# Optimization experiments

Hardware: AMD Instinct MI355X
Metric: run time of the kernel (lower is better)

Reference implementation:

```python
import jax, jax.numpy as jnp
import numpy as np

B, S, D, H = 8, 1024, 1024, 16
DK = D // H  # 64


def setup_inputs() -> dict:
    key = jax.random.key(0)
    ks = jax.random.split(key, 12)
    def w(k):
        return (jax.random.normal(k, (D, D), dtype=jnp.float32) * 0.02)
    def b(k):
        return (jax.random.normal(k, (D,), dtype=jnp.float32) * 0.02)
    return {
        "q": jax.random.normal(ks[0], (B, S, D), dtype=jnp.float32),
        "k": jax.random.normal(ks[1], (B, S, D), dtype=jnp.float32),
        "v": jax.random.normal(ks[2], (B, S, D), dtype=jnp.float32),
        "mask": jax.random.randint(ks[3], (B, 1, S, S), 0, 2, dtype=jnp.int32),
        "WQ_w": w(ks[4]), "WQ_b": b(ks[5]),
        "WK_w": w(ks[6]), "WK_b": b(ks[7]),
        "WV_w": w(ks[8]), "WV_b": b(ks[9]),
        "WO_w": w(ks[10]), "WO_b": b(ks[11]),
    }


def reference(q, k, v, mask, WQ_w, WQ_b, WK_w, WK_b, WV_w, WV_b, WO_w, WO_b):
    # nn.Linear: y = x @ W.T + b
    Q = (q @ WQ_w.T + WQ_b).reshape(B, S, H, DK)
    K = (k @ WK_w.T + WK_b).reshape(B, S, H, DK)
    V = (v @ WV_w.T + WV_b).reshape(B, S, H, DK)
    # scores: [B, H, Sq, Sk]
    scores = jnp.einsum("bqhd,bkhd->bhqk", Q, K) / jnp.sqrt(jnp.float32(DK))
    scores = jnp.where(mask == 0, jnp.float32(-1e9), scores)
    attn = jax.nn.softmax(scores, axis=-1)
    # dropout p=0.0 -> identity
    out = jnp.einsum("bhqk,bkhd->bqhd", attn, V).reshape(B, S, D)
    return out @ WO_w.T + WO_b
```

## Files before the change

### kernel.cpp

```cpp
#include <hip/hip_runtime.h>
#include <math.h>

typedef __bf16 bf16;
typedef __bf16 bf16x8 __attribute__((ext_vector_type(8)));
typedef __bf16 bf16x4 __attribute__((ext_vector_type(4)));
typedef float f32x2 __attribute__((ext_vector_type(2)));
typedef float f32x4 __attribute__((ext_vector_type(4)));
typedef float f32x16 __attribute__((ext_vector_type(16)));
typedef int i32x4 __attribute__((ext_vector_type(4)));

constexpr int B_ = 8, S_ = 1024, D_ = 1024, H_ = 16, DK_ = 64;
constexpr int M_ = B_ * S_;
constexpr size_t A8 = (size_t)1 << 23;
constexpr size_t W1 = (size_t)1 << 20;
constexpr float QSCALE = 0.18033688011112042f;

#if __has_builtin(__builtin_amdgcn_exp2f)
#define EXP2F(x) __builtin_amdgcn_exp2f(x)
#else
#define EXP2F(x) exp2f(x)
#endif
#if __has_builtin(__builtin_amdgcn_rcpf)
#define RCPF(x) __builtin_amdgcn_rcpf(x)
#else
#define RCPF(x) (1.0f / (x))
#endif

#define GAS(p) ((const __attribute__((address_space(1))) void*)(p))
#define LAS(p) ((__attribute__((address_space(3))) void*)(p))

__device__ __forceinline__ float xor32f(float v, int bpidx) {
    return __builtin_bit_cast(float,
        __builtin_amdgcn_ds_bpermute(bpidx, __builtin_bit_cast(int, v)));
}
__device__ __forceinline__ int xor32i(int v, int bpidx) {
    return __builtin_amdgcn_ds_bpermute(bpidx, v);
}
__device__ __forceinline__ int pack_bf16(bf16 lo, bf16 hi) {
    return (int)(unsigned)__builtin_bit_cast(unsigned short, lo)
         | ((int)(unsigned)__builtin_bit_cast(unsigned short, hi) << 16);
}

struct F4Q { f32x4 a, b, c, d; };


__global__ __launch_bounds__(256) void cvt_all(
    const float* __restrict__ q, const float* __restrict__ k,
    const float* __restrict__ v, const float* __restrict__ w0,
    const float* __restrict__ w1, const float* __restrict__ w2,
    const float* __restrict__ w3, bf16* __restrict__ dst)
{
    size_t e = ((size_t)blockIdx.x * 256 + threadIdx.x) * 8;
    const float* src;
    size_t off;
    if (e < 3 * A8) {
        int t = (int)(e >> 23);
        src = (t == 0) ? q : (t == 1) ? k : v;
        off = e & (A8 - 1);
    } else {
        size_t ew = e - 3 * A8;
        int t = (int)(ew >> 20);
        src = (t == 0) ? w0 : (t == 1) ? w1 : (t == 2) ? w2 : w3;
        off = ew & (W1 - 1);
    }
    float4 a = *(const float4*)(src + off);
    float4 b = *(const float4*)(src + off + 4);
    bf16x8 o = { (bf16)a.x, (bf16)a.y, (bf16)a.z, (bf16)a.w,
                 (bf16)b.x, (bf16)b.y, (bf16)b.z, (bf16)b.w };
    *(bf16x8*)(dst + e) = o;
}

__global__ __launch_bounds__(256) void mask_cvt(
    const int* __restrict__ mask, float* __restrict__ mf)
{
    const int bx = blockIdx.x;
    const int kt = bx & 15, qt = (bx >> 4) & 7, b = bx >> 7;
    const int tid = threadIdx.x;
    const int w = tid >> 6, lane = tid & 63;
    const int hi = lane >> 5, l31 = lane & 31;
    const int q = qt * 128 + w * 32 + l31;

    const int* src = mask + ((size_t)b << 20) + (size_t)q * 1024 + kt * 64 + hi * 4;
    float* dst = mf + (size_t)bx * 8192 + w * 2048 + lane * 4;
#pragma unroll
    for (int blk = 0; blk < 2; ++blk)
#pragma unroll
        for (int rr = 0; rr < 4; ++rr) {
            int4 m = *(const int4*)(src + blk * 32 + rr * 8);
            f32x4 o = { m.x ? 0.f : -1e9f, m.y ? 0.f : -1e9f,
                        m.z ? 0.f : -1e9f, m.w ? 0.f : -1e9f };
            *(f32x4*)(dst + (blk * 4 + rr) * 256) = o;
        }
}

__global__ __launch_bounds__(256) void qkv_gemm(
    const bf16* __restrict__ qb, const bf16* __restrict__ kb,
    const bf16* __restrict__ vb, const bf16* __restrict__ wq,
    const bf16* __restrict__ wk, const bf16* __restrict__ wv,
    const float* __restrict__ bq, const float* __restrict__ bk,
    const float* __restrict__ bv, bf16* __restrict__ Qp,
    bf16* __restrict__ Kp, bf16* __restrict__ Vp, float qscale)
{
    constexpr int K = 1024;
    __shared__ bf16 As[128 * 32];
    __shared__ bf16 Bs[128 * 32];

    const int bid = blockIdx.x;
    const int which = bid >> 9;
    const int gb = bid & 511;
    const bf16* X = which == 0 ? qb : which == 1 ? kb : vb;
    const bf16* W = which == 0 ? wq : which == 1 ? wk : wv;
    const float* bias = which == 0 ? bq : which == 1 ? bk : bv;
    bf16* outp = which == 0 ? Qp : which == 1 ? Kp : Vp;
    const float oscale = which == 0 ? qscale : 1.0f;

    const int tid  = threadIdx.x;
    const int lane = tid & 63;
    const int w    = tid >> 6;
    const int wm   = w & 1, wn = w >> 1;
    const int quad = lane >> 4, l15 = lane & 15;
    const int bm = (gb & 63) * 128, bn = (gb >> 6) * 128;

    f32x4 acc[4][4];
#pragma unroll
    for (int i = 0; i < 4; ++i)
#pragma unroll
        for (int j = 0; j < 4; ++j)
#pragma unroll
            for (int r = 0; r < 4; ++r) acc[i][j][r] = 0.f;

    const int lrow = lane >> 2;
    const int lcol = (lane & 3) * 8;

    for (int k0 = 0; k0 < K; k0 += 32) {
        __syncthreads();
#pragma unroll
        for (int i = 0; i < 2; ++i) {
            const int rbase = w * 16 + i * 64;
            __builtin_amdgcn_global_load_lds(
                GAS(X + (size_t)(bm + rbase + lrow) * K + k0 + lcol),
                LAS(As + rbase * 32), 16, 0, 0);
            __builtin_amdgcn_global_load_lds(
                GAS(W + (size_t)(bn + rbase + lrow) * K + k0 + lcol),
                LAS(Bs + rbase * 32), 16, 0, 0);
        }
        __syncthreads();

        bf16x8 a[4], b[4];
#pragma unroll
        for (int i = 0; i < 4; ++i)
            a[i] = *(const bf16x8*)(As + (wm * 64 + i * 16 + l15) * 32 + quad * 8);
#pragma unroll
        for (int j = 0; j < 4; ++j)
            b[j] = *(const bf16x8*)(Bs + (wn * 64 + j * 16 + l15) * 32 + quad * 8);
#pragma unroll
        for (int i = 0; i < 4; ++i)
#pragma unroll
            for (int j = 0; j < 4; ++j)
                acc[i][j] = __builtin_amdgcn_mfma_f32_16x16x32_bf16(
                    a[i], b[j], acc[i][j], 0, 0, 0);
    }

#pragma unroll
    for (int i = 0; i < 4; ++i) {
#pragma unroll
        for (int j = 0; j < 4; ++j) {
            const int n = bn + wn * 64 + j * 16 + l15;
            const float bs = bias[n];
            if (which == 2) {
                const int m0 = bm + wm * 64 + i * 16 + quad * 4;
                const int bb = m0 >> 10, s0 = m0 & 1023;
                const int h = n >> 6, dk = n & 63;
                bf16x4 o;
#pragma unroll
                for (int r = 0; r < 4; ++r) o[r] = (bf16)(acc[i][j][r] + bs);
                *(bf16x4*)(outp + (((size_t)(bb * 16 + h) * 64 + dk) << 10) + s0) = o;
            } else {
#pragma unroll
                for (int r = 0; r < 4; ++r) {
                    const int m = bm + wm * 64 + i * 16 + quad * 4 + r;
                    const int bb = m >> 10, s = m & 1023;
                    const int h = n >> 6, dk = n & 63;
                    outp[(((size_t)(bb * 16 + h)) * 1024 + s) * 64 + dk] =
                        (bf16)((acc[i][j][r] + bs) * oscale);
                }
            }
        }
    }
}

__global__ __launch_bounds__(256) void gemm_out(
    const bf16* __restrict__ X, const bf16* __restrict__ W,
    const float* __restrict__ bias, float* __restrict__ outv)
{
    constexpr int K = 1024;
    __shared__ bf16 As[128 * 32];
    __shared__ bf16 Bs[128 * 32];

    const int tid  = threadIdx.x;
    const int lane = tid & 63;
    const int w    = tid >> 6;
    const int wm   = w & 1, wn = w >> 1;
    const int quad = lane >> 4, l15 = lane & 15;
    const int bm = blockIdx.x * 128, bn = blockIdx.y * 128;

    f32x4 acc[4][4];
#pragma unroll
    for (int i = 0; i < 4; ++i)
#pragma unroll
        for (int j = 0; j < 4; ++j)
#pragma unroll
            for (int r = 0; r < 4; ++r) acc[i][j][r] = 0.f;

    const int lrow = lane >> 2;
    const int lcol = (lane & 3) * 8;

    for (int k0 = 0; k0 < K; k0 += 32) {
        __syncthreads();
#pragma unroll
        for (int i = 0; i < 2; ++i) {
            const int rbase = w * 16 + i * 64;
            __builtin_amdgcn_global_load_lds(
                GAS(X + (size_t)(bm + rbase + lrow) * K + k0 + lcol),
                LAS(As + rbase * 32), 16, 0, 0);
            __builtin_amdgcn_global_load_lds(
                GAS(W + (size_t)(bn + rbase + lrow) * K + k0 + lcol),
                LAS(Bs + rbase * 32), 16, 0, 0);
        }
        __syncthreads();

        bf16x8 a[4], b[4];
#pragma unroll
        for (int i = 0; i < 4; ++i)
            a[i] = *(const bf16x8*)(As + (wm * 64 + i * 16 + l15) * 32 + quad * 8);
#pragma unroll
        for (int j = 0; j < 4; ++j)
            b[j] = *(const bf16x8*)(Bs + (wn * 64 + j * 16 + l15) * 32 + quad * 8);
#pragma unroll
        for (int i = 0; i < 4; ++i)
#pragma unroll
            for (int j = 0; j < 4; ++j)
                acc[i][j] = __builtin_amdgcn_mfma_f32_16x16x32_bf16(
                    a[i], b[j], acc[i][j], 0, 0, 0);
    }

#pragma unroll
    for (int i = 0; i < 4; ++i)
#pragma unroll
        for (int j = 0; j < 4; ++j) {
            const int n = bn + wn * 64 + j * 16 + l15;
            const float bs = bias[n];
#pragma unroll
            for (int r = 0; r < 4; ++r) {
                const int m = bm + wm * 64 + i * 16 + quad * 4 + r;
                outv[(size_t)m * 1024 + n] = acc[i][j][r] + bs;
            }
        }
}

__global__ __launch_bounds__(256) void attn_mfma(
    const bf16* __restrict__ Q, const bf16* __restrict__ Kt,
    const bf16* __restrict__ Vt, const float* __restrict__ mf,
    bf16* __restrict__ out)
{
    __shared__ bf16 smem[2 * 2 * 4096];

    const int tid  = threadIdx.x;
    const int lane = tid & 63;
    const int w    = tid >> 6;
    const int hi   = lane >> 5, l31 = lane & 31;

    const int wid = (blockIdx.x & 7) * 128 + (blockIdx.x >> 3);
    const int qt = wid & 7;
    const int h  = (wid >> 3) & 15;
    const int b  = wid >> 7;

    const bf16* Qg  = Q + ((size_t)((b * H_ + h) * S_) + qt * 128 + w * 32) * DK_;
    const char* Kgh = (const char*)(Kt + (size_t)(b * H_ + h) * S_ * DK_);
    const char* Vgh = (const char*)(Vt + ((size_t)(b * H_ + h) << 16));
    const float* mtb = mf + (size_t)((b * 8 + qt) * 16) * 8192 + w * 2048 + lane * 4;

    const int tA = tid,        rA = tA >> 3, cA = (tA & 7) * 16;
    const int tB = 256 + tid,  rB = tB >> 3, cB = (tB & 7) * 16;
    const int kSrcA = rA * 128  + (cA ^ ((rA & 7) << 4));
    const int kSrcB = rB * 128  + (cB ^ ((rB & 7) << 4));
    const int vSrcA = rA * 2048 + (cA ^ ((rA & 7) << 4));
    const int vSrcB = rB * 2048 + (cB ^ ((rB & 7) << 4));

    auto stage = [&](int buf, int tkt) {
        bf16* Ks = smem + buf * 8192;
        bf16* Vs = Ks + 4096;
        const char* kg = Kgh + (size_t)tkt * 8192;
        const char* vg = Vgh + (size_t)tkt * 128;
        __builtin_amdgcn_global_load_lds(GAS(kg + kSrcA), LAS(Ks + w * 512),        16, 0, 0);
        __builtin_amdgcn_global_load_lds(GAS(kg + kSrcB), LAS(Ks + 2048 + w * 512), 16, 0, 0);
        __builtin_amdgcn_global_load_lds(GAS(vg + vSrcA), LAS(Vs + w * 512),        16, 0, 0);
        __builtin_amdgcn_global_load_lds(GAS(vg + vSrcB), LAS(Vs + 2048 + w * 512), 16, 0, 0);
    };

    stage(0, 0);

    bf16x8 qf[4];
#pragma unroll
    for (int ks = 0; ks < 4; ++ks)
        qf[ks] = *(const bf16x8*)(Qg + (size_t)l31 * 64 + ks * 16 + hi * 8);

    f32x4 mreg[8];
#pragma unroll
    for (int i = 0; i < 8; ++i) mreg[i] = *(const f32x4*)(mtb + i * 256);

    f32x16 O0, O1;
#pragma unroll
    for (int r = 0; r < 16; ++r) { O0[r] = 0.f; O1[r] = 0.f; }
    float mrow = -INFINITY, lrowv = 0.f;
    const int bpidx = (lane ^ 32) << 2;
    const int swz = (l31 & 7) << 4;

    __syncthreads();

#pragma unroll 2
    for (int kt = 0; kt < 16; ++kt) {
        const int buf = kt & 1;
        const bf16* Ks = smem + buf * 8192;
        const bf16* Vs = Ks + 4096;
        const char* KsB = (const char*)Ks;
        const char* VsB = (const char*)Vs;

        F4Q mq0 = { mreg[0], mreg[1], mreg[2], mreg[3] };
        F4Q mq1 = { mreg[4], mreg[5], mreg[6], mreg[7] };
        f32x16 acc0 = __builtin_bit_cast(f32x16, mq0);
        f32x16 acc1 = __builtin_bit_cast(f32x16, mq1);

        if (kt < 15) {
            const float* mkn = mtb + (size_t)(kt + 1) * 8192;
#pragma unroll
            for (int i = 0; i < 8; ++i) mreg[i] = *(const f32x4*)(mkn + i * 256);
        }

        if (kt + 1 < 16) stage(buf ^ 1, kt + 1);

#pragma unroll
        for (int ks = 0; ks < 4; ++ks) {
            const int cb = ks * 32 + hi * 16;
            bf16x8 k0 = *(const bf16x8*)(KsB + l31 * 128        + (cb ^ swz));
            bf16x8 k1 = *(const bf16x8*)(KsB + (l31 + 32) * 128 + (cb ^ swz));
            acc0 = __builtin_amdgcn_mfma_f32_32x32x16_bf16(k0, qf[ks], acc0, 0, 0, 0);
            acc1 = __builtin_amdgcn_mfma_f32_32x32x16_bf16(k1, qf[ks], acc1, 0, 0, 0);
        }

        float red[8];
#pragma unroll
        for (int i = 0; i < 8; ++i)
            red[i] = fmaxf(fmaxf(acc0[i], acc0[i + 8]), fmaxf(acc1[i], acc1[i + 8]));
#pragma unroll
        for (int i = 0; i < 4; ++i) red[i] = fmaxf(red[i], red[i + 4]);
        float mx = fmaxf(fmaxf(red[0], red[1]), fmaxf(red[2], red[3]));
        mx = fmaxf(mx, xor32f(mx, bpidx));

        if (__any(mx > mrow + 8.0f)) {
            const float mn = fmaxf(mrow, mx);
            const float alpha = EXP2F(mrow - mn);
            mrow = mn;
            lrowv *= alpha;
#pragma unroll
            for (int r = 0; r < 16; ++r) { O0[r] *= alpha; O1[r] *= alpha; }
        }

#pragma unroll
        for (int r = 0; r < 16; ++r) acc0[r] = EXP2F(acc0[r] - mrow);
#pragma unroll
        for (int r = 0; r < 16; ++r) acc1[r] = EXP2F(acc1[r] - mrow);

        int wd0[8], wd1[8];
        float ps = 0.f;
#pragma unroll
        for (int s = 0; s < 8; ++s) {
            bf16 e0 = (bf16)acc0[2 * s], o0 = (bf16)acc0[2 * s + 1];
            bf16 e1 = (bf16)acc1[2 * s], o1 = (bf16)acc1[2 * s + 1];
            ps += (float)e0 + (float)o0 + (float)e1 + (float)o1;
            wd0[s] = pack_bf16(e0, o0);
            wd1[s] = pack_bf16(e1, o1);
        }
        ps += xor32f(ps, bpidx);
        lrowv += ps;

#pragma unroll
        for (int ks = 0; ks < 4; ++ks) {
            const int s0 = (ks & 1) * 4;
            int p0, p1, p2, p3;
            if (ks < 2) { p0 = wd0[s0]; p1 = wd0[s0 + 1]; p2 = wd0[s0 + 2]; p3 = wd0[s0 + 3]; }
            else        { p0 = wd1[s0]; p1 = wd1[s0 + 1]; p2 = wd1[s0 + 2]; p3 = wd1[s0 + 3]; }
            const int rx = xor32i(hi ? p0 : p2, bpidx);
            const int ry = xor32i(hi ? p1 : p3, bpidx);
            i32x4 pw = { hi ? rx : p0, hi ? ry : p1, hi ? p2 : rx, hi ? p3 : ry };
            bf16x8 pa = __builtin_bit_cast(bf16x8, pw);

            const int cb = ks * 32 + hi * 16;
            bf16x8 v0 = *(const bf16x8*)(VsB + l31 * 128        + (cb ^ swz));
            bf16x8 v1 = *(const bf16x8*)(VsB + (l31 + 32) * 128 + (cb ^ swz));
            O0 = __builtin_amdgcn_mfma_f32_32x32x16_bf16(v0, pa, O0, 0, 0, 0);
            O1 = __builtin_amdgcn_mfma_f32_32x32x16_bf16(v1, pa, O1, 0, 0, 0);
        }
        __syncthreads();
    }

    const float rinv = RCPF(lrowv);
    bf16* og = out + ((size_t)b * S_ + qt * 128 + w * 32 + l31) * D_ + h * DK_;
#pragma unroll
    for (int rr = 0; rr < 4; ++rr) {
        bf16x4 o0 = { (bf16)(O0[rr * 4 + 0] * rinv), (bf16)(O0[rr * 4 + 1] * rinv),
                      (bf16)(O0[rr * 4 + 2] * rinv), (bf16)(O0[rr * 4 + 3] * rinv) };
        bf16x4 o1 = { (bf16)(O1[rr * 4 + 0] * rinv), (bf16)(O1[rr * 4 + 1] * rinv),
                      (bf16)(O1[rr * 4 + 2] * rinv), (bf16)(O1[rr * 4 + 3] * rinv) };
        *(bf16x4*)(og + rr * 8 + hi * 4)      = o0;
        *(bf16x4*)(og + 32 + rr * 8 + hi * 4) = o1;
    }
}

extern "C" void kernel_launch(void* const* d_in, const int* in_sizes, int n_in,
                              void* d_out, int out_size, void* d_ws, size_t ws_size,
                              hipStream_t stream) {
    const float* q    = (const float*)d_in[0];
    const float* k    = (const float*)d_in[1];
    const float* v    = (const float*)d_in[2];
    const int*   mask = (const int*)d_in[3];
    const float* WQw  = (const float*)d_in[4];
    const float* WQb  = (const float*)d_in[5];
    const float* WKw  = (const float*)d_in[6];
    const float* WKb  = (const float*)d_in[7];
    const float* WVw  = (const float*)d_in[8];
    const float* WVb  = (const float*)d_in[9];
    const float* WOw  = (const float*)d_in[10];
    const float* WOb  = (const float*)d_in[11];

    bf16* ws = (bf16*)d_ws;
    bf16* qb  = ws;
    bf16* kb  = qb + A8;
    bf16* vb  = kb + A8;
    bf16* wqb = vb + A8;
    bf16* wkb = wqb + W1;
    bf16* wvb = wkb + W1;
    bf16* wob = wvb + W1;
    bf16* Qp  = wob + W1;
    bf16* Kp  = Qp + A8;
    bf16* Vp  = Kp + A8;
    float* maskf = (float*)qb;
    bf16* AO     = vb;

    cvt_all<<<dim3(14336), 256, 0, stream>>>(q, k, v, WQw, WKw, WVw, WOw, ws);

    qkv_gemm<<<dim3(1536), 256, 0, stream>>>(qb, kb, vb, wqb, wkb, wvb,
                                             WQb, WKb, WVb, Qp, Kp, Vp, QSCALE);

    mask_cvt<<<dim3(1024), 256, 0, stream>>>(mask, maskf);

    attn_mfma<<<dim3(1024), 256, 0, stream>>>(Qp, Kp, Vp, maskf, AO);

    gemm_out<<<dim3(M_ / 128, D_ / 128), 256, 0, stream>>>(AO, wob, WOb, (float*)d_out);
}
```

Measured before the change: 350.1 us.

## Fuse fp32-to-bf16 activation conversion into QKV GEMM via swizzled fp32 LDS tiles

Removes the separate pass that converted q, k and v to bf16. The QKV GEMM now loads fp32 activation tiles straight into LDS using an XOR-swizzled layout, and converts them to bf16 when it reads the fragments. A separate small kernel still converts the weights. The workspace is re-laid out so the mask and attention output get their own buffers, and the mask conversion is launched before the GEMM. This saves a full read and write of the activations, but the GEMM now reads twice as many bytes per A tile, uses more LDS and does extra conversion work in its inner loop.

```diff
diff --git a/kernel.cpp b/kernel.cpp
--- a/kernel.cpp
+++ b/kernel.cpp
@@ -44,25 +44,15 @@
 struct F4Q { f32x4 a, b, c, d; };
 
 
-__global__ __launch_bounds__(256) void cvt_all(
-    const float* __restrict__ q, const float* __restrict__ k,
-    const float* __restrict__ v, const float* __restrict__ w0,
-    const float* __restrict__ w1, const float* __restrict__ w2,
-    const float* __restrict__ w3, bf16* __restrict__ dst)
+__global__ __launch_bounds__(256) void wcvt(
+    const float* __restrict__ w0, const float* __restrict__ w1,
+    const float* __restrict__ w2, const float* __restrict__ w3,
+    bf16* __restrict__ dst)
 {
     size_t e = ((size_t)blockIdx.x * 256 + threadIdx.x) * 8;
-    const float* src;
-    size_t off;
-    if (e < 3 * A8) {
-        int t = (int)(e >> 23);
-        src = (t == 0) ? q : (t == 1) ? k : v;
-        off = e & (A8 - 1);
-    } else {
-        size_t ew = e - 3 * A8;
-        int t = (int)(ew >> 20);
-        src = (t == 0) ? w0 : (t == 1) ? w1 : (t == 2) ? w2 : w3;
-        off = ew & (W1 - 1);
-    }
+    int t = (int)(e >> 20);
+    const float* src = (t == 0) ? w0 : (t == 1) ? w1 : (t == 2) ? w2 : w3;
+    size_t off = e & (W1 - 1);
     float4 a = *(const float4*)(src + off);
     float4 b = *(const float4*)(src + off + 4);
     bf16x8 o = { (bf16)a.x, (bf16)a.y, (bf16)a.z, (bf16)a.w,
@@ -94,21 +84,21 @@
 }
 
 __global__ __launch_bounds__(256) void qkv_gemm(
-    const bf16* __restrict__ qb, const bf16* __restrict__ kb,
-    const bf16* __restrict__ vb, const bf16* __restrict__ wq,
+    const float* __restrict__ qx, const float* __restrict__ kx,
+    const float* __restrict__ vx, const bf16* __restrict__ wq,
     const bf16* __restrict__ wk, const bf16* __restrict__ wv,
     const float* __restrict__ bq, const float* __restrict__ bk,
     const float* __restrict__ bv, bf16* __restrict__ Qp,
     bf16* __restrict__ Kp, bf16* __restrict__ Vp, float qscale)
 {
     constexpr int K = 1024;
-    __shared__ bf16 As[128 * 32];
+    __shared__ float Asf[128 * 32];
     __shared__ bf16 Bs[128 * 32];
 
     const int bid = blockIdx.x;
     const int which = bid >> 9;
     const int gb = bid & 511;
-    const bf16* X = which == 0 ? qb : which == 1 ? kb : vb;
+    const float* X = which == 0 ? qx : which == 1 ? kx : vx;
     const bf16* W = which == 0 ? wq : which == 1 ? wk : wv;
     const float* bias = which == 0 ? bq : which == 1 ? bk : bv;
     bf16* outp = which == 0 ? Qp : which == 1 ? Kp : Vp;
@@ -129,27 +119,39 @@
 #pragma unroll
             for (int r = 0; r < 4; ++r) acc[i][j][r] = 0.f;
 
+    const int lr   = lane >> 3;
+    const int acol = ((lane & 7) * 4) ^ ((lr & 3) << 3);
     const int lrow = lane >> 2;
     const int lcol = (lane & 3) * 8;
 
     for (int k0 = 0; k0 < K; k0 += 32) {
         __syncthreads();
 #pragma unroll
+        for (int i = 0; i < 4; ++i) {
+            const int ra = i * 32 + w * 8;
+            __builtin_amdgcn_global_load_lds(
+                GAS(X + (size_t)(bm + ra + lr) * K + k0 + acol),
+                LAS(Asf + ra * 32), 16, 0, 0);
+        }
+#pragma unroll
         for (int i = 0; i < 2; ++i) {
-            const int rbase = w * 16 + i * 64;
+            const int rb = w * 16 + i * 64;
             __builtin_amdgcn_global_load_lds(
-                GAS(X + (size_t)(bm + rbase + lrow) * K + k0 + lcol),
-                LAS(As + rbase * 32), 16, 0, 0);
-            __builtin_amdgcn_global_load_lds(
-                GAS(W + (size_t)(bn + rbase + lrow) * K + k0 + lcol),
-                LAS(Bs + rbase * 32), 16, 0, 0);
+                GAS(W + (size_t)(bn + rb + lrow) * K + k0 + lcol),
+                LAS(Bs + rb * 32), 16, 0, 0);
         }
         __syncthreads();
 
         bf16x8 a[4], b[4];
 #pragma unroll
-        for (int i = 0; i < 4; ++i)
-            a[i] = *(const bf16x8*)(As + (wm * 64 + i * 16 + l15) * 32 + quad * 8);
+        for (int i = 0; i < 4; ++i) {
+            const int r = wm * 64 + i * 16 + l15;
+            const int idx = r * 32 + ((quad * 8) ^ ((r & 3) << 3));
+            f32x4 lo = *(const f32x4*)(Asf + idx);
+            f32x4 hi = *(const f32x4*)(Asf + idx + 4);
+            a[i] = (bf16x8){ (bf16)lo[0], (bf16)lo[1], (bf16)lo[2], (bf16)lo[3],
+                             (bf16)hi[0], (bf16)hi[1], (bf16)hi[2], (bf16)hi[3] };
+        }
 #pragma unroll
         for (int j = 0; j < 4; ++j)
             b[j] = *(const bf16x8*)(Bs + (wn * 64 + j * 16 + l15) * 32 + quad * 8);
@@ -433,27 +435,24 @@
     const float* WOw  = (const float*)d_in[10];
     const float* WOb  = (const float*)d_in[11];
 
-    bf16* ws = (bf16*)d_ws;
-    bf16* qb  = ws;
-    bf16* kb  = qb + A8;
-    bf16* vb  = kb + A8;
-    bf16* wqb = vb + A8;
+    bf16* ws  = (bf16*)d_ws;
+    bf16* wqb = ws;
     bf16* wkb = wqb + W1;
     bf16* wvb = wkb + W1;
     bf16* wob = wvb + W1;
     bf16* Qp  = wob + W1;
     bf16* Kp  = Qp + A8;
     bf16* Vp  = Kp + A8;
-    float* maskf = (float*)qb;
-    bf16* AO     = vb;
-
-    cvt_all<<<dim3(14336), 256, 0, stream>>>(q, k, v, WQw, WKw, WVw, WOw, ws);
-
-    qkv_gemm<<<dim3(1536), 256, 0, stream>>>(qb, kb, vb, wqb, wkb, wvb,
+    float* maskf = (float*)(Vp + A8);
+    bf16* AO  = (bf16*)(maskf + A8);
+
+    wcvt<<<dim3(2048), 256, 0, stream>>>(WQw, WKw, WVw, WOw, wqb);
+
+    mask_cvt<<<dim3(1024), 256, 0, stream>>>(mask, maskf);
+
+    qkv_gemm<<<dim3(1536), 256, 0, stream>>>(q, k, v, wqb, wkb, wvb,
                                              WQb, WKb, WVb, Qp, Kp, Vp, QSCALE);
 
-    mask_cvt<<<dim3(1024), 256, 0, stream>>>(mask, maskf);
-
     attn_mfma<<<dim3(1024), 256, 0, stream>>>(Qp, Kp, Vp, maskf, AO);
 
     gemm_out<<<dim3(M_ / 128, D_ / 128), 256, 0, stream>>>(AO, wob, WOb, (float*)d_out);
```

Result: slower. 365.1 us (+4.3%).
